# Kernel optimization log

Hardware: AMD Instinct MI355X
Metric: run time of the kernel (lower is better)

The kernel has to match this reference:

```python
import jax, jax.numpy as jnp
import numpy as np

N_Q = 8
DIM = 2 ** N_Q          # 256
DEGREE = 3
ANSATZ_LAYERS = 2


def gelu(x):
    return jax.nn.gelu(x, approximate=False)


def layer_norm(x, g, b, eps=1e-5):
    mu = x.mean(-1, keepdims=True)
    v = x.var(-1, keepdims=True)
    return (x - mu) / jnp.sqrt(v + eps) * g + b


def apply_ry(state, theta, w, n):
    # state: (B, 2^n) complex64, theta: (B,) per-element angle
    half = theta * 0.5
    c, s = jnp.cos(half), jnp.sin(half)
    U = jnp.stack([jnp.stack([c, -s], -1), jnp.stack([s, c], -1)], -2).astype(state.dtype)
    L, R = 2 ** w, 2 ** (n - 1 - w)
    st = state.reshape(-1, L, 2, R)
    st = jnp.einsum('bij,bljr->blir', U, st)
    return st.reshape(state.shape)


def apply_crx(state, theta, c, t, n):
    # controlled-RX(theta), control wire c, target wire t (batched angles)
    half = theta * 0.5
    cs = jnp.cos(half).astype(state.dtype)
    ms = (-1j) * jnp.sin(half).astype(state.dtype)
    Rx = jnp.stack([jnp.stack([cs, ms], -1), jnp.stack([ms, cs], -1)], -2)  # (B,2,2)
    a, b = min(c, t), max(c, t)
    A, M, R = 2 ** a, 2 ** (b - a - 1), 2 ** (n - 1 - b)
    st = state.reshape(-1, A, 2, M, 2, R)
    if c < t:
        sub = st[:, :, 1]                              # control bit = 1 slice, (B,A,M,2,R)
        sub = jnp.einsum('bij,bamjr->bamir', Rx, sub)
        st = st.at[:, :, 1].set(sub)
    else:
        sub = st[:, :, :, :, 1]                        # (B,A,2,M,R)
        sub = jnp.einsum('bij,bajmr->baimr', Rx, sub)
        st = st.at[:, :, :, :, 1].set(sub)
    return st.reshape(state.shape)


def sim14(state, params, n, layers):
    # Sim et al. 2019 circuit 14: RY layer, CRX ring, RY layer, reversed CRX ring (4n params/layer)
    idx = 0
    for _ in range(layers):
        for q in range(n):
            state = apply_ry(state, params[:, idx + q], q, n)
        idx += n
        for q in range(n):
            state = apply_crx(state, params[:, idx + q], q, (q + 1) % n, n)
        idx += n
        for q in range(n):
            state = apply_ry(state, params[:, idx + q], q, n)
        idx += n
        for q in range(n):
            state = apply_crx(state, params[:, idx + q], q, (q - 1) % n, n)
        idx += n
    return state


def pauli_expvals(psi, n):
    # [<X_0..X_{n-1}>, <Y_0..>, <Z_0..>] for batched pure states psi: (B, 2^n)
    xs, ys, zs = [], [], []
    for w in range(n):
        L, R = 2 ** w, 2 ** (n - 1 - w)
        s = psi.reshape(-1, L, 2, R)
        s0, s1 = s[:, :, 0], s[:, :, 1]
        cross = (jnp.conj(s0) * s1).sum((1, 2))
        xs.append(2.0 * jnp.real(cross))
        ys.append(2.0 * jnp.imag(cross))
        zs.append((jnp.abs(s0) ** 2 - jnp.abs(s1) ** 2).sum((1, 2)))
    return jnp.stack(xs + ys + zs, axis=1).astype(jnp.float32)


def dwsep_conv(x, dw_w, dw_b, pw_w, pw_b, gn_g, gn_b, dilation):
    # depthwise-separable conv1d + GroupNorm(8) + GELU; x: (B, C, T)
    k = dw_w.shape[-1]
    pad = (k - 1) * dilation // 2
    y = jax.lax.conv_general_dilated(
        x, dw_w, window_strides=(1,), padding=[(pad, pad)], rhs_dilation=(dilation,),
        feature_group_count=x.shape[1], dimension_numbers=('NCH', 'OIH', 'NCH'))
    y = y + dw_b[None, :, None]
    y = jnp.einsum('oc,bct->bot', pw_w, y) + pw_b[None, :, None]
    B, C, T = y.shape
    g = y.reshape(B, 8, C // 8, T)
    mu = g.mean((2, 3), keepdims=True)
    var = g.var((2, 3), keepdims=True)
    y = ((g - mu) / jnp.sqrt(var + 1e-5)).reshape(B, C, T)
    return gelu(y * gn_g[None, :, None] + gn_b[None, :, None])


def setup_inputs() -> dict:
    key = jax.random.key(0)
    ks = iter(jax.random.split(key, 64))
    rn = lambda *s: jax.random.normal(next(ks), s, jnp.float32) * 0.05
    ru = lambda *s: jax.random.uniform(next(ks), s, dtype=jnp.float32)
    inp = dict(
        x=jax.random.normal(next(ks), (16, 363, 180), jnp.float32),
        net_w=rn(12, 15, 8), net_b=rn(12, 8),
        dwa_w=rn(96, 1, 7), dwa_b=rn(96), pwa_w=rn(96, 96), pwa_b=rn(96),
        gna_g=jnp.ones(96, jnp.float32), gna_b=jnp.zeros(96, jnp.float32),
        dwb_w=rn(96, 1, 7), dwb_b=rn(96), pwb_w=rn(96, 96), pwb_b=rn(96),
        gnb_g=jnp.ones(96, jnp.float32), gnb_b=jnp.zeros(96, jnp.float32),
        dwc_w=rn(96, 1, 7), dwc_b=rn(96), pwc_w=rn(96, 96), pwc_b=rn(96),
        gnc_g=jnp.ones(96, jnp.float32), gnc_b=jnp.zeros(96, jnp.float32),
        merge_w=rn(288, 128), merge_b=rn(128),
        merge_ln_g=jnp.ones(128, jnp.float32), merge_ln_b=jnp.zeros(128, jnp.float32),
        qproj_w=rn(128, 64), qproj_b=rn(64),
        poly_coeffs=ru(4), qff_params=ru(32),
        mix_re=ru(363), mix_im=ru(363),
        qout_w=rn(24, 128), qout_b=rn(128),
        fc_w=rn(78, 64), fc_b=rn(64),
        fus1_w=rn(192, 128), fus1_b=rn(128),
        fus_ln_g=jnp.ones(128, jnp.float32), fus_ln_b=jnp.zeros(128, jnp.float32),
        fus2_w=rn(128, 64), fus2_b=rn(64),
    )
    return inp


def reference(x, net_w, net_b, dwa_w, dwa_b, pwa_w, pwa_b, gna_g, gna_b,
              dwb_w, dwb_b, pwb_w, pwb_b, gnb_g, gnb_b,
              dwc_w, dwc_b, pwc_w, pwc_b, gnc_g, gnc_b,
              merge_w, merge_b, merge_ln_g, merge_ln_b,
              qproj_w, qproj_b, poly_coeffs, qff_params, mix_re, mix_im,
              qout_w, qout_b, fc_w, fc_b,
              fus1_w, fus1_b, fus_ln_g, fus_ln_b, fus2_w, fus2_b):
    B, T, C = x.shape
    # --- network projection: 12 contiguous networks of 15 ROIs -> d_net=8 each ---
    h = jnp.einsum('btki,kid->btkd', x.reshape(B, T, 12, 15), net_w) + net_b
    h = gelu(h).reshape(B, T, 96)
    # --- multiscale depthwise-separable convs ---
    ht = h.transpose(0, 2, 1)  # (B,96,T)
    a = dwsep_conv(ht, dwa_w, dwa_b, pwa_w, pwa_b, gna_g, gna_b, 1)
    b = dwsep_conv(ht, dwb_w, dwb_b, pwb_w, pwb_b, gnb_g, gnb_b, 4)
    c = dwsep_conv(ht, dwc_w, dwc_b, pwc_w, pwc_b, gnc_g, gnc_b, 16)
    cat = jnp.concatenate([a, b, c], axis=1).transpose(0, 2, 1)  # (B,T,288)
    h = gelu(layer_norm(cat @ merge_w + merge_b, merge_ln_g, merge_ln_b))  # (B,T,128)
    # --- QSVT quantum temporal mixing ---
    tp = jax.nn.sigmoid(h @ qproj_w + qproj_b) * (2.0 * np.pi)  # (B,T,64) rotation angles
    tp = tp.reshape(B * T, -1)
    base = jnp.zeros((B * T, DIM), jnp.complex64).at[:, 0].set(1.0)
    pc = poly_coeffs.astype(jnp.complex64)
    state = base
    acc = pc[0] * base
    for d in range(1, DEGREE + 1):
        state = sim14(state, tp, N_Q, ANSATZ_LAYERS)
        acc = acc + pc[d] * state
    acc = acc.reshape(B, T, DIM)
    mix = (mix_re + 1j * mix_im).astype(jnp.complex64)[:T]
    mixed = jnp.einsum('t,btd->bd', mix, acc)           # temporal mixing
    norm = jnp.linalg.norm(mixed, axis=1, keepdims=True)
    psi = mixed / (norm + 1e-9)
    psi = sim14(psi, jnp.broadcast_to(qff_params[None, :], (B, qff_params.shape[0])), N_Q, 1)
    exps = pauli_expvals(psi, N_Q)                      # (B,24)
    temporal = exps @ qout_w + qout_b                   # (B,128)
    # --- FC fingerprint ---
    xm = x - x.mean(1, keepdims=True)
    std = jnp.maximum(jnp.std(x, axis=1, keepdims=True, ddof=1), 1e-8)
    xn = xm / std
    corr = jnp.einsum('btc,btd->bcd', xn, xn) / (T - 1)
    bm = corr.reshape(B, 12, 15, 12, 15).mean((2, 4))   # (B,12,12) network-block means
    iu0, iu1 = jnp.triu_indices(12)
    fc_vec = bm[:, iu0, iu1]                            # (B,78)
    fc = gelu(fc_vec @ fc_w + fc_b)                     # (B,64)
    # --- fusion ---
    fused = jnp.concatenate([temporal, fc], axis=1)
    out = gelu(layer_norm(fused @ fus1_w + fus1_b, fus_ln_g, fus_ln_b)) @ fus2_w + fus2_b
    return out  # (B,64)
```

## Files before the change

kernel.cpp:

```cpp
#include <hip/hip_runtime.h>
#include <math.h>

#define NB 16
#define NT 363
#define NC 180
#define SZF 557568
#define NROW 5808

__device__ __forceinline__ float gelu_f(float x) {
  return 0.5f * x * (1.0f + erff(x * 0.7071067811865475244f));
}


template<int CTRL>
__device__ __forceinline__ float dppf(float x) {
  return __int_as_float(__builtin_amdgcn_update_dpp(
      0, __float_as_int(x), CTRL, 0xF, 0xF, true));
}

template<int LB>
__device__ __forceinline__ float lx(float x) {
  if constexpr (LB == 0) return dppf<0xB1>(x);
  else if constexpr (LB == 1) return dppf<0x4E>(x);
  else if constexpr (LB == 2) return __shfl_xor(x, 4);
  else return __shfl_xor(x, 8);
}

template<int P>
__device__ __forceinline__ void ry_local(float* re, float* im, float c, float s) {
#pragma unroll
  for (int j = 0; j < 16; ++j) {
    if ((j & (1 << P)) == 0) {
      int k = j | (1 << P);
      float r0 = re[j], i0 = im[j], r1 = re[k], i1 = im[k];
      re[j] = fmaf(c, r0, -s * r1); im[j] = fmaf(c, i0, -s * i1);
      re[k] = fmaf(s, r0,  c * r1); im[k] = fmaf(s, i0,  c * i1);
    }
  }
}

template<int LB>
__device__ __forceinline__ void ry_lane(float* re, float* im, float c, float s, int lane) {
  float sg = (lane & (1 << LB)) ? s : -s;
#pragma unroll
  for (int j = 0; j < 16; ++j) {
    float br = lx<LB>(re[j]);
    float bi = lx<LB>(im[j]);
    re[j] = fmaf(c, re[j], sg * br);
    im[j] = fmaf(c, im[j], sg * bi);
  }
}

template<int Q, int P>
__device__ __forceinline__ void crx_ll(float* re, float* im, float cs, float sn) {
#pragma unroll
  for (int j = 0; j < 16; ++j) {
    if ((j & (1 << Q)) && !(j & (1 << P))) {
      int k = j | (1 << P);
      float r0 = re[j], i0 = im[j], r1 = re[k], i1 = im[k];
      re[j] = fmaf(cs, r0,  sn * i1); im[j] = fmaf(cs, i0, -sn * r1);
      re[k] = fmaf(cs, r1,  sn * i0); im[k] = fmaf(cs, i1, -sn * r0);
    }
  }
}

template<int LBQ, int P>
__device__ __forceinline__ void crx_nl(float* re, float* im, float cs, float sn, int lane) {
  if (lane & (1 << LBQ)) {
#pragma unroll
    for (int j = 0; j < 16; ++j) {
      if ((j & (1 << P)) == 0) {
        int k = j | (1 << P);
        float r0 = re[j], i0 = im[j], r1 = re[k], i1 = im[k];
        re[j] = fmaf(cs, r0,  sn * i1); im[j] = fmaf(cs, i0, -sn * r1);
        re[k] = fmaf(cs, r1,  sn * i0); im[k] = fmaf(cs, i1, -sn * r0);
      }
    }
  }
}

template<int Q, int LBP>
__device__ __forceinline__ void crx_ln(float* re, float* im, float cs, float sn) {
#pragma unroll
  for (int j = 0; j < 16; ++j) {
    if (j & (1 << Q)) {
      float br = lx<LBP>(re[j]);
      float bi = lx<LBP>(im[j]);
      re[j] = fmaf(cs, re[j],  sn * bi);
      im[j] = fmaf(cs, im[j], -sn * br);
    }
  }
}

template<int LBQ, int LBP>
__device__ __forceinline__ void crx_nn(float* re, float* im, float cs, float sn, int lane) {
  bool ctl = (lane & (1 << LBQ)) != 0;
#pragma unroll
  for (int j = 0; j < 16; ++j) {
    float br = lx<LBP>(re[j]);
    float bi = lx<LBP>(im[j]);
    if (ctl) {
      re[j] = fmaf(cs, re[j],  sn * bi);
      im[j] = fmaf(cs, im[j], -sn * br);
    }
  }
}

__device__ __forceinline__ void qlayer(float* re, float* im,
                                       const float2* ang, int lane) {
  float2 a;
  a = ang[0];  ry_lane<3>(re, im, a.x, a.y, lane);
  a = ang[1];  ry_lane<2>(re, im, a.x, a.y, lane);
  a = ang[2];  ry_lane<1>(re, im, a.x, a.y, lane);
  a = ang[3];  ry_lane<0>(re, im, a.x, a.y, lane);
  a = ang[4];  ry_local<3>(re, im, a.x, a.y);
  a = ang[5];  ry_local<2>(re, im, a.x, a.y);
  a = ang[6];  ry_local<1>(re, im, a.x, a.y);
  a = ang[7];  ry_local<0>(re, im, a.x, a.y);
  a = ang[8];  crx_nn<3, 2>(re, im, a.x, a.y, lane);
  a = ang[9];  crx_nn<2, 1>(re, im, a.x, a.y, lane);
  a = ang[10]; crx_nn<1, 0>(re, im, a.x, a.y, lane);
  a = ang[11]; crx_nl<0, 3>(re, im, a.x, a.y, lane);
  a = ang[12]; crx_ll<3, 2>(re, im, a.x, a.y);
  a = ang[13]; crx_ll<2, 1>(re, im, a.x, a.y);
  a = ang[14]; crx_ll<1, 0>(re, im, a.x, a.y);
  a = ang[15]; crx_ln<0, 3>(re, im, a.x, a.y);
  a = ang[16]; ry_lane<3>(re, im, a.x, a.y, lane);
  a = ang[17]; ry_lane<2>(re, im, a.x, a.y, lane);
  a = ang[18]; ry_lane<1>(re, im, a.x, a.y, lane);
  a = ang[19]; ry_lane<0>(re, im, a.x, a.y, lane);
  a = ang[20]; ry_local<3>(re, im, a.x, a.y);
  a = ang[21]; ry_local<2>(re, im, a.x, a.y);
  a = ang[22]; ry_local<1>(re, im, a.x, a.y);
  a = ang[23]; ry_local<0>(re, im, a.x, a.y);
  a = ang[24]; crx_nl<3, 0>(re, im, a.x, a.y, lane);
  a = ang[25]; crx_nn<2, 3>(re, im, a.x, a.y, lane);
  a = ang[26]; crx_nn<1, 2>(re, im, a.x, a.y, lane);
  a = ang[27]; crx_nn<0, 1>(re, im, a.x, a.y, lane);
  a = ang[28]; crx_ln<3, 0>(re, im, a.x, a.y);
  a = ang[29]; crx_ll<2, 3>(re, im, a.x, a.y);
  a = ang[30]; crx_ll<1, 2>(re, im, a.x, a.y);
  a = ang[31]; crx_ll<0, 1>(re, im, a.x, a.y);
}

template<int P>
__device__ __forceinline__ void ryg(float* re, float* im, float c, float s, int lane) {
  if constexpr (P >= 2) {
    constexpr int mask = 1 << (P - 2);
    float sg = ((lane >> (P - 2)) & 1) ? s : -s;
#pragma unroll
    for (int j = 0; j < 4; ++j) {
      float br = __shfl_xor(re[j], mask);
      float bi = __shfl_xor(im[j], mask);
      re[j] = fmaf(c, re[j], sg * br);
      im[j] = fmaf(c, im[j], sg * bi);
    }
  } else {
#pragma unroll
    for (int k = 0; k < 2; ++k) {
      const int a = (P == 0) ? 2 * k : k;
      const int b = (P == 0) ? a + 1 : a + 2;
      float r0 = re[a], i0 = im[a], r1 = re[b], i1 = im[b];
      re[a] = fmaf(c, r0, -s * r1); im[a] = fmaf(c, i0, -s * i1);
      re[b] = fmaf(s, r0,  c * r1); im[b] = fmaf(s, i0,  c * i1);
    }
  }
}

template<int PC, int PT>
__device__ __forceinline__ void crxg(float* re, float* im, float cs, float sn, int lane) {
  if constexpr (PT >= 2) {
    constexpr int mask = 1 << (PT - 2);
#pragma unroll
    for (int j = 0; j < 4; ++j) {
      float br = __shfl_xor(re[j], mask);
      float bi = __shfl_xor(im[j], mask);
      bool ctrl;
      if constexpr (PC >= 2) ctrl = ((lane >> (PC - 2)) & 1) != 0;
      else                   ctrl = ((j >> PC) & 1) != 0;
      if (ctrl) {
        float nr = fmaf(cs, re[j],  sn * bi);
        float ni = fmaf(cs, im[j], -sn * br);
        re[j] = nr; im[j] = ni;
      }
    }
  } else {
#pragma unroll
    for (int k = 0; k < 2; ++k) {
      const int a = (PT == 0) ? 2 * k : k;
      const int b = (PT == 0) ? a + 1 : a + 2;
      bool ctrl;
      if constexpr (PC >= 2) ctrl = ((lane >> (PC - 2)) & 1) != 0;
      else                   ctrl = ((a >> PC) & 1) != 0;
      if (ctrl) {
        float r0 = re[a], i0 = im[a], r1 = re[b], i1 = im[b];
        re[a] = fmaf(cs, r0,  sn * i1); im[a] = fmaf(cs, i0, -sn * r1);
        re[b] = fmaf(cs, r1,  sn * i0); im[b] = fmaf(cs, i1, -sn * r0);
      }
    }
  }
}

__device__ __forceinline__ void sim14_layer(float* re, float* im,
                                            const float* Cr, const float* Sr, int lane) {
#define ARY1(q, pi) ryg<7-(q)>(re, im, Cr[pi], Sr[pi], lane)
#define ACX1(cq, tq, pi) crxg<7-(cq), 7-(tq)>(re, im, Cr[pi], Sr[pi], lane)
  ARY1(0,0); ARY1(1,1); ARY1(2,2); ARY1(3,3); ARY1(4,4); ARY1(5,5); ARY1(6,6); ARY1(7,7);
  ACX1(0,1,8); ACX1(1,2,9); ACX1(2,3,10); ACX1(3,4,11); ACX1(4,5,12); ACX1(5,6,13); ACX1(6,7,14); ACX1(7,0,15);
  ARY1(0,16); ARY1(1,17); ARY1(2,18); ARY1(3,19); ARY1(4,20); ARY1(5,21); ARY1(6,22); ARY1(7,23);
  ACX1(0,7,24); ACX1(1,0,25); ACX1(2,1,26); ACX1(3,2,27); ACX1(4,3,28); ACX1(5,4,29); ACX1(6,5,30); ACX1(7,6,31);
#undef ARY1
#undef ACX1
}

struct CorrSM { float mu[180]; float inv[180]; float S[NT * 12]; float fcv[78]; };
struct EmdwSM {
  float xs[NT * 15];
  float nwL[120], nbL[8];
  float hrow[8][368];
  float wL[3][8][8];
  float bL[3][8];
};
union EDSM { EmdwSM e; CorrSM c; };

__global__ __launch_bounds__(256) void k_emdw(const float* __restrict__ x,
    const float* __restrict__ nw, const float* __restrict__ nb,
    const float* __restrict__ wa, const float* __restrict__ ba,
    const float* __restrict__ wb, const float* __restrict__ bb,
    const float* __restrict__ wc, const float* __restrict__ bc,
    float* __restrict__ y1base,
    const float* __restrict__ fcw, const float* __restrict__ fcb,
    float* __restrict__ fusedG) {
  __shared__ EDSM sm;
  int b = blockIdx.x, kg = blockIdx.y, tid = threadIdx.x;
  if (kg < 12) {
    for (int i = tid; i < 120; i += 256) sm.e.nwL[i] = nw[kg * 120 + i];
    for (int i = tid; i < 8; i += 256) sm.e.nbL[i] = nb[kg * 8 + i];
    for (int i = tid; i < 168; i += 256) {
      int z = i / 56, r = i % 56, d = r / 7, k = r % 7;
      const float* w = (z == 0) ? wa : ((z == 1) ? wb : wc);
      sm.e.wL[z][d][k] = w[(kg * 8 + d) * 7 + k];
    }
    for (int i = tid; i < 24; i += 256) {
      int z = i / 8, d = i % 8;
      const float* bias = (z == 0) ? ba : ((z == 1) ? bb : bc);
      sm.e.bL[z][d] = bias[kg * 8 + d];
    }
    for (int i = tid; i < NT * 15; i += 256) {
      int t = i / 15, u = i % 15;
      sm.e.xs[i] = x[((size_t)b * NT + t) * NC + kg * 15 + u];
    }
    __syncthreads();
    for (int i = tid; i < 8 * NT; i += 256) {
      int t = i % NT, d = i / NT;
      float acc2 = sm.e.nbL[d];
#pragma unroll
      for (int u = 0; u < 15; ++u) acc2 = fmaf(sm.e.xs[t * 15 + u], sm.e.nwL[u * 8 + d], acc2);
      sm.e.hrow[d][t] = gelu_f(acc2);
    }
    __syncthreads();
    for (int i = tid; i < 8 * NT; i += 256) {
      int t = i % NT, d = i / NT;
      int c = kg * 8 + d;
      float a0 = sm.e.bL[0][d], a1 = sm.e.bL[1][d], a2 = sm.e.bL[2][d];
#pragma unroll
      for (int k = 0; k < 7; ++k) {
        int i1 = t + (k - 3);
        int i4 = t + (k - 3) * 4;
        int i16 = t + (k - 3) * 16;
        if (i1 >= 0 && i1 < NT)  a0 = fmaf(sm.e.hrow[d][i1],  sm.e.wL[0][d][k], a0);
        if (i4 >= 0 && i4 < NT)  a1 = fmaf(sm.e.hrow[d][i4],  sm.e.wL[1][d][k], a1);
        if (i16 >= 0 && i16 < NT) a2 = fmaf(sm.e.hrow[d][i16], sm.e.wL[2][d][k], a2);
      }
      size_t base = ((size_t)b * 96 + c) * NT + t;
      y1base[base] = a0;
      y1base[SZF + base] = a1;
      y1base[2 * SZF + base] = a2;
    }
  } else {
    if (tid < 180) {
      float s = 0;
      const float* px = x + (size_t)b * NT * NC + tid;
      for (int t = 0; t < NT; ++t) s += px[t * NC];
      float mu = s / 363.0f;
      float q = 0;
      for (int t = 0; t < NT; ++t) { float d = px[t * NC] - mu; q = fmaf(d, d, q); }
      float sd = sqrtf(q / 362.0f);
      sd = fmaxf(sd, 1e-8f);
      sm.c.mu[tid] = mu; sm.c.inv[tid] = 1.0f / sd;
    }
    __syncthreads();
    for (int t = tid; t < NT; t += 256) {
      const float* px = x + (size_t)(b * NT + t) * NC;
#pragma unroll
      for (int i = 0; i < 12; ++i) {
        float s = 0;
#pragma unroll
        for (int u = 0; u < 15; ++u) {
          int cidx = i * 15 + u;
          s += (px[cidx] - sm.c.mu[cidx]) * sm.c.inv[cidx];
        }
        sm.c.S[t * 12 + i] = s;
      }
    }
    __syncthreads();
    if (tid < 78) {
      int i = 0, rem = tid;
      while (rem >= 12 - i) { rem -= 12 - i; ++i; }
      int j = i + rem;
      float acc = 0;
      for (int t = 0; t < NT; ++t) acc = fmaf(sm.c.S[t * 12 + i], sm.c.S[t * 12 + j], acc);
      sm.c.fcv[tid] = acc * (1.0f / (225.0f * 362.0f));
    }
    __syncthreads();
    if (tid < 64) {
      float v = fcb[tid];
#pragma unroll
      for (int k = 0; k < 78; ++k) v = fmaf(sm.c.fcv[k], fcw[k * 64 + tid], v);
      fusedG[b * 192 + 128 + tid] = gelu_f(v);
    }
  }
}

__global__ __launch_bounds__(256) void k_pw(const float* __restrict__ y1base,
    const float* __restrict__ wA, const float* __restrict__ wB, const float* __restrict__ wC,
    const float* __restrict__ bA, const float* __restrict__ bB, const float* __restrict__ bC,
    float* __restrict__ y2base) {
  int b = blockIdx.x, tile = blockIdx.y, z = blockIdx.z, tid = threadIdx.x;
  const float* pw_w = (z == 0) ? wA : ((z == 1) ? wB : wC);
  const float* pw_b = (z == 0) ? bA : ((z == 1) ? bB : bC);
  const float* y1 = y1base + (size_t)z * SZF;
  float* y2 = y2base + (size_t)z * SZF;
  int t0 = tile * 64;
  __shared__ float y1t[96 * 64];
  __shared__ float pwL[96 * 97];
  for (int i = tid; i < 96 * 96; i += 256) {
    int o = i / 96, cc = i % 96;
    pwL[o * 97 + cc] = pw_w[i];
  }
  for (int i = tid; i < 96 * 64; i += 256) {
    int cc = i >> 6, t = i & 63;
    int tt = t0 + t;
    y1t[i] = (tt < NT) ? y1[(b * 96 + cc) * NT + tt] : 0.0f;
  }
  __syncthreads();
  int o16 = tid >> 4, t4 = (tid & 15) * 4;
  for (int pass = 0; pass < 6; ++pass) {
    int o = pass * 16 + o16;
    float bias = pw_b[o];
    float a0 = bias, a1 = bias, a2 = bias, a3 = bias;
    const float* wrow = &pwL[o * 97];
#pragma unroll 4
    for (int cc = 0; cc < 96; ++cc) {
      const float4 vy = *reinterpret_cast<const float4*>(&y1t[cc * 64 + t4]);
      float w = wrow[cc];
      a0 = fmaf(w, vy.x, a0); a1 = fmaf(w, vy.y, a1);
      a2 = fmaf(w, vy.z, a2); a3 = fmaf(w, vy.w, a3);
    }
    int base = (b * 96 + o) * NT;
    int t = t0 + t4;
    if (t + 3 < NT) {
      y2[base + t] = a0; y2[base + t + 1] = a1; y2[base + t + 2] = a2; y2[base + t + 3] = a3;
    } else {
      if (t < NT) y2[base + t] = a0;
      if (t + 1 < NT) y2[base + t + 1] = a1;
      if (t + 2 < NT) y2[base + t + 2] = a2;
      if (t + 3 < NT) y2[base + t + 3] = a3;
    }
  }
}

__global__ __launch_bounds__(256) void k_gnstat(const float* __restrict__ y2base,
                                                float* __restrict__ muG,
                                                float* __restrict__ rsG) {
  int b = blockIdx.x, g = blockIdx.y, z = blockIdx.z, tid = threadIdx.x;
  __shared__ float red[256];
  const float* base = y2base + (size_t)z * SZF + (b * 96 + g * 12) * NT;
  float s = 0;
  for (int i = tid; i < 12 * NT; i += 256) s += base[i];
  red[tid] = s; __syncthreads();
  for (int st = 128; st > 0; st >>= 1) { if (tid < st) red[tid] += red[tid + st]; __syncthreads(); }
  float mu = red[0] / 4356.0f;
  __syncthreads();
  float q = 0;
  for (int i = tid; i < 12 * NT; i += 256) { float d = base[i] - mu; q = fmaf(d, d, q); }
  red[tid] = q; __syncthreads();
  for (int st = 128; st > 0; st >>= 1) { if (tid < st) red[tid] += red[tid + st]; __syncthreads(); }
  if (tid == 0) {
    float var = red[0] / 4356.0f;
    muG[(z * NB + b) * 8 + g] = mu;
    rsG[(z * NB + b) * 8 + g] = rsqrtf(var + 1e-5f);
  }
}

__global__ __launch_bounds__(256) void k_gnapply(const float* __restrict__ y2base,
    const float* __restrict__ muG, const float* __restrict__ rsG,
    const float* __restrict__ gA, const float* __restrict__ gB, const float* __restrict__ gC,
    const float* __restrict__ bA, const float* __restrict__ bB, const float* __restrict__ bC,
    float* __restrict__ cat) {
  int b = blockIdx.x, tile = blockIdx.y, z = blockIdx.z, tid = threadIdx.x;
  const float* gng = (z == 0) ? gA : ((z == 1) ? gB : gC);
  const float* gnb = (z == 0) ? bA : ((z == 1) ? bB : bC);
  const float* y2 = y2base + (size_t)z * SZF;
  int t0 = tile * 64;
  __shared__ float yL[96 * 65];
  __shared__ float muL[8], rsL[8];
  if (tid < 8) { muL[tid] = muG[(z * NB + b) * 8 + tid]; rsL[tid] = rsG[(z * NB + b) * 8 + tid]; }
  for (int i = tid; i < 96 * 64; i += 256) {
    int cc = i >> 6, t = i & 63;
    int tt = t0 + t;
    yL[cc * 65 + t] = (tt < NT) ? y2[(b * 96 + cc) * NT + tt] : 0.0f;
  }
  __syncthreads();
  for (int i = tid; i < 64 * 96; i += 256) {
    int tt = i / 96, cc = i % 96;
    int t = t0 + tt;
    if (t < NT) {
      int g = cc / 12;
      float v = (yL[cc * 65 + tt] - muL[g]) * rsL[g] * gng[cc] + gnb[cc];
      cat[((size_t)b * NT + t) * 288 + z * 96 + cc] = gelu_f(v);
    }
  }
}

__global__ __launch_bounds__(256) void k_merge(const float* __restrict__ cat,
    const float* __restrict__ mw, const float* __restrict__ mb,
    const float* __restrict__ lng, const float* __restrict__ lnb,
    const float* __restrict__ qw, const float* __restrict__ qb,
    float2* __restrict__ angG) {
  int blk = blockIdx.x, tid = threadIdx.x;
  __shared__ float catL[8][288];
  __shared__ float vL[8][129];
  __shared__ float hL[8][129];
  __shared__ float muS[8], rsS[8];
  for (int i = tid; i < 8 * 288; i += 256) {
    int r = i / 288, k = i % 288;
    catL[r][k] = cat[((size_t)blk * 8 + r) * 288 + k];
  }
  __syncthreads();
  int jj = tid & 127, rg = tid >> 7;
  float bias = mb[jj];
  float acc[4] = {bias, bias, bias, bias};
  for (int k = 0; k < 288; ++k) {
    float w = mw[k * 128 + jj];
#pragma unroll
    for (int r = 0; r < 4; ++r) acc[r] = fmaf(catL[rg * 4 + r][k], w, acc[r]);
  }
#pragma unroll
  for (int r = 0; r < 4; ++r) vL[rg * 4 + r][jj] = acc[r];
  __syncthreads();
  if (tid < 8) {
    float s = 0;
    for (int k = 0; k < 128; ++k) s += vL[tid][k];
    float mu = s / 128.0f;
    float q = 0;
    for (int k = 0; k < 128; ++k) { float d = vL[tid][k] - mu; q = fmaf(d, d, q); }
    muS[tid] = mu;
    rsS[tid] = rsqrtf(q / 128.0f + 1e-5f);
  }
  __syncthreads();
  float g = lng[jj], bb2 = lnb[jj];
#pragma unroll
  for (int r = 0; r < 4; ++r) {
    int row = rg * 4 + r;
    float h = (acc[r] - muS[row]) * rsS[row] * g + bb2;
    hL[row][jj] = gelu_f(h);
  }
  __syncthreads();
  int o = tid & 63;
  int r0 = (tid >> 6) * 2;
  for (int rr = 0; rr < 2; ++rr) {
    int row = r0 + rr;
    float u = qb[o];
    for (int k = 0; k < 128; ++k) u = fmaf(hL[row][k], qw[k * 64 + o], u);
    float tp = 6.2831853071795864769f / (1.0f + expf(-u));
    float hf = tp * 0.5f;
    int grow = blk * 8 + row;
    angG[(size_t)grow * 64 + o] = make_float2(cosf(hf), sinf(hf));
  }
}

__global__ __launch_bounds__(64) void k_quantum(const float2* __restrict__ angG,
                                                const float* __restrict__ pc4,
                                                float* __restrict__ accG) {
  const int lane = threadIdx.x;
  const int g = lane >> 4;
  const int ll = lane & 15;
  const int row0 = blockIdx.x * 4;
  __shared__ float2 angL[4][66];
#pragma unroll
  for (int q = 0; q < 4; ++q)
    angL[q][lane] = angG[(size_t)(row0 + q) * 64 + lane];
  __syncthreads();
  float p0 = pc4[0], p1 = pc4[1], p2 = pc4[2], p3 = pc4[3];
  float re[16], im[16];
#pragma unroll
  for (int j = 0; j < 16; ++j) { re[j] = 0.0f; im[j] = 0.0f; }
  if (ll == 0) re[0] = p3;
  const float2* ang = &angL[g][0];
  for (int rep = 0; rep < 3; ++rep) {
    qlayer(re, im, ang, lane);
    qlayer(re, im, ang + 32, lane);
    float pc = (rep == 0) ? p2 : (rep == 1) ? p1 : p0;
    if (ll == 0) re[0] += pc;
  }
  int row = row0 + g;
  float4* dst = reinterpret_cast<float4*>(accG + ((size_t)row * 256 + ll * 16) * 2);
#pragma unroll
  for (int h = 0; h < 8; ++h)
    dst[h] = make_float4(re[2 * h], im[2 * h], re[2 * h + 1], im[2 * h + 1]);
}

__global__ __launch_bounds__(256) void k_mix1(const float* __restrict__ accG,
                                              const float* __restrict__ mr,
                                              const float* __restrict__ mi,
                                              float* __restrict__ part) {
  int b = blockIdx.x, ch = blockIdx.y, d = threadIdx.x;
  int t0 = ch * 33;
  float sr = 0, si = 0;
  for (int i = 0; i < 33; ++i) {
    int t = t0 + i;
    const float2 a = *reinterpret_cast<const float2*>(accG + (size_t)((b * NT + t) * 256 + d) * 2);
    float m_r = mr[t], m_i = mi[t];
    sr = fmaf(m_r, a.x, fmaf(-m_i, a.y, sr));
    si = fmaf(m_r, a.y, fmaf(m_i, a.x, si));
  }
  float2* o = reinterpret_cast<float2*>(part + (size_t)((b * 11 + ch) * 256 + d) * 2);
  *o = make_float2(sr, si);
}

__global__ __launch_bounds__(256) void k_tail(const float* __restrict__ part,
    const float* __restrict__ qff,
    const float* __restrict__ qout_w, const float* __restrict__ qout_b,
    const float* __restrict__ fusedG,
    const float* __restrict__ w1, const float* __restrict__ b1,
    const float* __restrict__ lng, const float* __restrict__ lnb,
    const float* __restrict__ w2, const float* __restrict__ b2,
    float* __restrict__ out) {
  int b = blockIdx.x, tid = threadIdx.x;
  __shared__ float psiL[256][2];
  __shared__ float red[256];
  __shared__ float qcL[32], qsL[32], exps[24];
  __shared__ float tL[128], cL[64], hL[128];
  {
    float sr = 0, si = 0;
    for (int ch = 0; ch < 11; ++ch) {
      const float2 a = *reinterpret_cast<const float2*>(part + (size_t)((b * 11 + ch) * 256 + tid) * 2);
      sr += a.x; si += a.y;
    }
    psiL[tid][0] = sr; psiL[tid][1] = si;
    red[tid] = sr * sr + si * si;
  }
  if (tid < 32) { float h = qff[tid] * 0.5f; qcL[tid] = cosf(h); qsL[tid] = sinf(h); }
  __syncthreads();
  for (int s2 = 128; s2 > 0; s2 >>= 1) { if (tid < s2) red[tid] += red[tid + s2]; __syncthreads(); }
  float inv = 1.0f / (sqrtf(red[0]) + 1e-9f);
  __syncthreads();
  if (tid < 64) {
    int lane = tid;
    float re[4], im[4];
#pragma unroll
    for (int j = 0; j < 4; ++j) {
      re[j] = psiL[lane * 4 + j][0] * inv;
      im[j] = psiL[lane * 4 + j][1] * inv;
    }
    sim14_layer(re, im, qcL, qsL, lane);
#pragma unroll
    for (int j = 0; j < 4; ++j) { psiL[lane * 4 + j][0] = re[j]; psiL[lane * 4 + j][1] = im[j]; }
  }
  __syncthreads();
  if (tid < 64) {
    int lane = tid;
    for (int w = 0; w < 8; ++w) {
      int p = 7 - w;
      float cr = 0, ci = 0, z = 0;
#pragma unroll
      for (int k = 0; k < 2; ++k) {
        int pr = lane + k * 64;
        int lowmask = (1 << p) - 1;
        int i0 = ((pr >> p) << (p + 1)) | (pr & lowmask);
        int i1 = i0 | (1 << p);
        float r0 = psiL[i0][0], I0 = psiL[i0][1], r1 = psiL[i1][0], I1 = psiL[i1][1];
        cr += r0 * r1 + I0 * I1;
        ci += r0 * I1 - I0 * r1;
        z += r0 * r0 + I0 * I0 - r1 * r1 - I1 * I1;
      }
      for (int off = 32; off > 0; off >>= 1) {
        cr += __shfl_down(cr, off);
        ci += __shfl_down(ci, off);
        z  += __shfl_down(z, off);
      }
      if (lane == 0) { exps[w] = 2.0f * cr; exps[8 + w] = 2.0f * ci; exps[16 + w] = z; }
    }
  }
  __syncthreads();
  if (tid < 128) {
    float v = qout_b[tid];
#pragma unroll
    for (int k = 0; k < 24; ++k) v = fmaf(exps[k], qout_w[k * 128 + tid], v);
    tL[tid] = v;
  } else if (tid < 192) {
    cL[tid - 128] = fusedG[b * 192 + 128 + (tid - 128)];
  }
  __syncthreads();
  float v = 0.0f;
  if (tid < 128) {
    v = b1[tid];
    for (int k = 0; k < 128; ++k) v = fmaf(tL[k], w1[k * 128 + tid], v);
    for (int k = 0; k < 64; ++k)  v = fmaf(cL[k], w1[(128 + k) * 128 + tid], v);
    red[tid] = v;
  }
  __syncthreads();
  for (int s = 64; s > 0; s >>= 1) { if (tid < s) red[tid] += red[tid + s]; __syncthreads(); }
  float mu = red[0] / 128.0f;
  __syncthreads();
  float dv = v - mu;
  if (tid < 128) red[tid] = dv * dv;
  __syncthreads();
  for (int s = 64; s > 0; s >>= 1) { if (tid < s) red[tid] += red[tid + s]; __syncthreads(); }
  float var = red[0] / 128.0f;
  if (tid < 128) hL[tid] = gelu_f(dv * rsqrtf(var + 1e-5f) * lng[tid] + lnb[tid]);
  __syncthreads();
  if (tid < 64) {
    float o = b2[tid];
    for (int k = 0; k < 128; ++k) o = fmaf(hL[k], w2[k * 64 + tid], o);
    out[b * 64 + tid] = o;
  }
}

extern "C" void kernel_launch(void* const* d_in, const int* in_sizes, int n_in,
                              void* d_out, int out_size, void* d_ws, size_t ws_size,
                              hipStream_t stream) {
  const float* x       = (const float*)d_in[0];
  const float* net_w   = (const float*)d_in[1];
  const float* net_b   = (const float*)d_in[2];
  const float* dwa_w   = (const float*)d_in[3];
  const float* dwa_b   = (const float*)d_in[4];
  const float* pwa_w   = (const float*)d_in[5];
  const float* pwa_b   = (const float*)d_in[6];
  const float* gna_g   = (const float*)d_in[7];
  const float* gna_b   = (const float*)d_in[8];
  const float* dwb_w   = (const float*)d_in[9];
  const float* dwb_b   = (const float*)d_in[10];
  const float* pwb_w   = (const float*)d_in[11];
  const float* pwb_b   = (const float*)d_in[12];
  const float* gnb_g   = (const float*)d_in[13];
  const float* gnb_b   = (const float*)d_in[14];
  const float* dwc_w   = (const float*)d_in[15];
  const float* dwc_b   = (const float*)d_in[16];
  const float* pwc_w   = (const float*)d_in[17];
  const float* pwc_b   = (const float*)d_in[18];
  const float* gnc_g   = (const float*)d_in[19];
  const float* gnc_b   = (const float*)d_in[20];
  const float* merge_w = (const float*)d_in[21];
  const float* merge_b = (const float*)d_in[22];
  const float* mlng    = (const float*)d_in[23];
  const float* mlnb    = (const float*)d_in[24];
  const float* qproj_w = (const float*)d_in[25];
  const float* qproj_b = (const float*)d_in[26];
  const float* poly    = (const float*)d_in[27];
  const float* qff     = (const float*)d_in[28];
  const float* mix_re  = (const float*)d_in[29];
  const float* mix_im  = (const float*)d_in[30];
  const float* qout_w  = (const float*)d_in[31];
  const float* qout_b  = (const float*)d_in[32];
  const float* fc_w    = (const float*)d_in[33];
  const float* fc_b    = (const float*)d_in[34];
  const float* fus1_w  = (const float*)d_in[35];
  const float* fus1_b  = (const float*)d_in[36];
  const float* flng    = (const float*)d_in[37];
  const float* flnb    = (const float*)d_in[38];
  const float* fus2_w  = (const float*)d_in[39];
  const float* fus2_b  = (const float*)d_in[40];
  float* out = (float*)d_out;

  float* W = (float*)d_ws;
  float* y1b_  = W;
  float* cat   = W;
  float* y2b_  = W + 3 * (size_t)SZF;
  float* acc   = W;
  float2* angG = (float2*)(W + 6 * (size_t)SZF);
  float* muG   = W + 6 * (size_t)SZF + 743424;
  float* rsG   = muG + 512;
  float* part  = rsG + 512;
  float* fused = part + 90112;

  k_emdw<<<dim3(NB, 13), 256, 0, stream>>>(x, net_w, net_b,
      dwa_w, dwa_b, dwb_w, dwb_b, dwc_w, dwc_b, y1b_, fc_w, fc_b, fused);
  k_pw<<<dim3(NB, 6, 3), 256, 0, stream>>>(y1b_, pwa_w, pwb_w, pwc_w, pwa_b, pwb_b, pwc_b, y2b_);
  k_gnstat<<<dim3(NB, 8, 3), 256, 0, stream>>>(y2b_, muG, rsG);
  k_gnapply<<<dim3(NB, 6, 3), 256, 0, stream>>>(y2b_, muG, rsG,
      gna_g, gnb_g, gnc_g, gna_b, gnb_b, gnc_b, cat);
  k_merge<<<726, 256, 0, stream>>>(cat, merge_w, merge_b, mlng, mlnb,
      qproj_w, qproj_b, angG);
  k_quantum<<<NROW / 4, 64, 0, stream>>>(angG, poly, acc);
  k_mix1<<<dim3(NB, 11), 256, 0, stream>>>(acc, mix_re, mix_im, part);
  k_tail<<<NB, 256, 0, stream>>>(part, qff, qout_w, qout_b, fused,
                                 fus1_w, fus1_b, flng, flnb, fus2_w, fus2_b, out);
}
```

Measured before the change: 316.8 us.

## Fuse group-norm stats into pointwise conv and temporal mixing into quantum kernel

GroupNorm statistics are now built in the pointwise conv kernel as per-group sum and sum-of-squares using wave shuffles and atomics, with buffers zeroed in the first kernel. This removes the separate stats kernel and its re-read of y2. The quantum kernel also applies the complex temporal mixing weight and reduces four time steps in-register before writing partial sums, so the full per-timestep state buffer and the mix kernel go away. In exchange, the tail kernel sums 91 partials instead of 11, variance uses E[x^2]-mu^2, which is less numerically stable, and atomic summation order is nondeterministic.

```diff
diff --git a/kernel.cpp b/kernel.cpp
--- a/kernel.cpp
+++ b/kernel.cpp
@@ -230,7 +230,8 @@
     const float* __restrict__ wc, const float* __restrict__ bc,
     float* __restrict__ y1base,
     const float* __restrict__ fcw, const float* __restrict__ fcb,
-    float* __restrict__ fusedG) {
+    float* __restrict__ fusedG,
+    float* __restrict__ statS, float* __restrict__ statQ) {
   __shared__ EDSM sm;
   int b = blockIdx.x, kg = blockIdx.y, tid = threadIdx.x;
   if (kg < 12) {
@@ -278,6 +279,11 @@
       y1base[2 * SZF + base] = a2;
     }
   } else {
+    if (tid < 24) {
+      int z = tid / 8, g = tid % 8;
+      statS[(z * NB + b) * 8 + g] = 0.0f;
+      statQ[(z * NB + b) * 8 + g] = 0.0f;
+    }
     if (tid < 180) {
       float s = 0;
       const float* px = x + (size_t)b * NT * NC + tid;
@@ -325,7 +331,8 @@
 __global__ __launch_bounds__(256) void k_pw(const float* __restrict__ y1base,
     const float* __restrict__ wA, const float* __restrict__ wB, const float* __restrict__ wC,
     const float* __restrict__ bA, const float* __restrict__ bB, const float* __restrict__ bC,
-    float* __restrict__ y2base) {
+    float* __restrict__ y2base,
+    float* __restrict__ statS, float* __restrict__ statQ) {
   int b = blockIdx.x, tile = blockIdx.y, z = blockIdx.z, tid = threadIdx.x;
   const float* pw_w = (z == 0) ? wA : ((z == 1) ? wB : wC);
   const float* pw_b = (z == 0) ? bA : ((z == 1) ? bB : bC);
@@ -367,34 +374,26 @@
       if (t + 2 < NT) y2[base + t + 2] = a2;
       if (t + 3 < NT) y2[base + t + 3] = a3;
     }
-  }
-}
-
-__global__ __launch_bounds__(256) void k_gnstat(const float* __restrict__ y2base,
-                                                float* __restrict__ muG,
-                                                float* __restrict__ rsG) {
-  int b = blockIdx.x, g = blockIdx.y, z = blockIdx.z, tid = threadIdx.x;
-  __shared__ float red[256];
-  const float* base = y2base + (size_t)z * SZF + (b * 96 + g * 12) * NT;
-  float s = 0;
-  for (int i = tid; i < 12 * NT; i += 256) s += base[i];
-  red[tid] = s; __syncthreads();
-  for (int st = 128; st > 0; st >>= 1) { if (tid < st) red[tid] += red[tid + st]; __syncthreads(); }
-  float mu = red[0] / 4356.0f;
-  __syncthreads();
-  float q = 0;
-  for (int i = tid; i < 12 * NT; i += 256) { float d = base[i] - mu; q = fmaf(d, d, q); }
-  red[tid] = q; __syncthreads();
-  for (int st = 128; st > 0; st >>= 1) { if (tid < st) red[tid] += red[tid + st]; __syncthreads(); }
-  if (tid == 0) {
-    float var = red[0] / 4356.0f;
-    muG[(z * NB + b) * 8 + g] = mu;
-    rsG[(z * NB + b) * 8 + g] = rsqrtf(var + 1e-5f);
+    float s = 0.0f, q = 0.0f;
+    if (t < NT)     { s += a0; q = fmaf(a0, a0, q); }
+    if (t + 1 < NT) { s += a1; q = fmaf(a1, a1, q); }
+    if (t + 2 < NT) { s += a2; q = fmaf(a2, a2, q); }
+    if (t + 3 < NT) { s += a3; q = fmaf(a3, a3, q); }
+#pragma unroll
+    for (int m = 1; m <= 8; m <<= 1) {
+      s += __shfl_xor(s, m);
+      q += __shfl_xor(q, m);
+    }
+    if ((tid & 15) == 0) {
+      int g = o / 12;
+      atomicAdd(&statS[(z * NB + b) * 8 + g], s);
+      atomicAdd(&statQ[(z * NB + b) * 8 + g], q);
+    }
   }
 }
 
 __global__ __launch_bounds__(256) void k_gnapply(const float* __restrict__ y2base,
-    const float* __restrict__ muG, const float* __restrict__ rsG,
+    const float* __restrict__ statS, const float* __restrict__ statQ,
     const float* __restrict__ gA, const float* __restrict__ gB, const float* __restrict__ gC,
     const float* __restrict__ bA, const float* __restrict__ bB, const float* __restrict__ bC,
     float* __restrict__ cat) {
@@ -405,7 +404,14 @@
   int t0 = tile * 64;
   __shared__ float yL[96 * 65];
   __shared__ float muL[8], rsL[8];
-  if (tid < 8) { muL[tid] = muG[(z * NB + b) * 8 + tid]; rsL[tid] = rsG[(z * NB + b) * 8 + tid]; }
+  if (tid < 8) {
+    float S = statS[(z * NB + b) * 8 + tid];
+    float Q = statQ[(z * NB + b) * 8 + tid];
+    float mu = S / 4356.0f;
+    float var = Q / 4356.0f - mu * mu;
+    muL[tid] = mu;
+    rsL[tid] = rsqrtf(fmaxf(var, 0.0f) + 1e-5f);
+  }
   for (int i = tid; i < 96 * 64; i += 256) {
     int cc = i >> 6, t = i & 63;
     int tt = t0 + t;
@@ -482,15 +488,21 @@
 
 __global__ __launch_bounds__(64) void k_quantum(const float2* __restrict__ angG,
                                                 const float* __restrict__ pc4,
-                                                float* __restrict__ accG) {
+                                                const float* __restrict__ mr,
+                                                const float* __restrict__ mi,
+                                                float* __restrict__ part) {
   const int lane = threadIdx.x;
   const int g = lane >> 4;
   const int ll = lane & 15;
-  const int row0 = blockIdx.x * 4;
+  const int b = blockIdx.x;
+  const int i = blockIdx.y;
   __shared__ float2 angL[4][66];
 #pragma unroll
-  for (int q = 0; q < 4; ++q)
-    angL[q][lane] = angG[(size_t)(row0 + q) * 64 + lane];
+  for (int q = 0; q < 4; ++q) {
+    int t = i * 4 + q;
+    if (t >= NT) t = NT - 1;
+    angL[q][lane] = angG[(size_t)(b * NT + t) * 64 + lane];
+  }
   __syncthreads();
   float p0 = pc4[0], p1 = pc4[1], p2 = pc4[2], p3 = pc4[3];
   float re[16], im[16];
@@ -504,29 +516,30 @@
     float pc = (rep == 0) ? p2 : (rep == 1) ? p1 : p0;
     if (ll == 0) re[0] += pc;
   }
-  int row = row0 + g;
-  float4* dst = reinterpret_cast<float4*>(accG + ((size_t)row * 256 + ll * 16) * 2);
-#pragma unroll
-  for (int h = 0; h < 8; ++h)
-    dst[h] = make_float4(re[2 * h], im[2 * h], re[2 * h + 1], im[2 * h + 1]);
-}
-
-__global__ __launch_bounds__(256) void k_mix1(const float* __restrict__ accG,
-                                              const float* __restrict__ mr,
-                                              const float* __restrict__ mi,
-                                              float* __restrict__ part) {
-  int b = blockIdx.x, ch = blockIdx.y, d = threadIdx.x;
-  int t0 = ch * 33;
-  float sr = 0, si = 0;
-  for (int i = 0; i < 33; ++i) {
-    int t = t0 + i;
-    const float2 a = *reinterpret_cast<const float2*>(accG + (size_t)((b * NT + t) * 256 + d) * 2);
-    float m_r = mr[t], m_i = mi[t];
-    sr = fmaf(m_r, a.x, fmaf(-m_i, a.y, sr));
-    si = fmaf(m_r, a.y, fmaf(m_i, a.x, si));
-  }
-  float2* o = reinterpret_cast<float2*>(part + (size_t)((b * 11 + ch) * 256 + d) * 2);
-  *o = make_float2(sr, si);
+  {
+    int t = i * 4 + g;
+    float m_r = 0.0f, m_i = 0.0f;
+    if (t < NT) { m_r = mr[t]; m_i = mi[t]; }
+#pragma unroll
+    for (int j = 0; j < 16; ++j) {
+      float r = re[j], v = im[j];
+      re[j] = m_r * r - m_i * v;
+      im[j] = m_r * v + m_i * r;
+    }
+#pragma unroll
+    for (int j = 0; j < 16; ++j) {
+      re[j] += __shfl_xor(re[j], 16);
+      im[j] += __shfl_xor(im[j], 16);
+      re[j] += __shfl_xor(re[j], 32);
+      im[j] += __shfl_xor(im[j], 32);
+    }
+  }
+  if (g == 0) {
+    float4* dst = reinterpret_cast<float4*>(part + ((size_t)(b * 91 + i) * 256 + ll * 16) * 2);
+#pragma unroll
+    for (int h = 0; h < 8; ++h)
+      dst[h] = make_float4(re[2 * h], im[2 * h], re[2 * h + 1], im[2 * h + 1]);
+  }
 }
 
 __global__ __launch_bounds__(256) void k_tail(const float* __restrict__ part,
@@ -543,9 +556,10 @@
   __shared__ float qcL[32], qsL[32], exps[24];
   __shared__ float tL[128], cL[64], hL[128];
   {
+    const float2* pv = reinterpret_cast<const float2*>(part) + (size_t)(b * 91) * 256 + tid;
     float sr = 0, si = 0;
-    for (int ch = 0; ch < 11; ++ch) {
-      const float2 a = *reinterpret_cast<const float2*>(part + (size_t)((b * 11 + ch) * 256 + tid) * 2);
+    for (int i = 0; i < 91; ++i) {
+      float2 a = pv[(size_t)i * 256];
       sr += a.x; si += a.y;
     }
     psiL[tid][0] = sr; psiL[tid][1] = si;
@@ -678,23 +692,21 @@
   float* y1b_  = W;
   float* cat   = W;
   float* y2b_  = W + 3 * (size_t)SZF;
-  float* acc   = W;
   float2* angG = (float2*)(W + 6 * (size_t)SZF);
-  float* muG   = W + 6 * (size_t)SZF + 743424;
-  float* rsG   = muG + 512;
-  float* part  = rsG + 512;
-  float* fused = part + 90112;
+  float* statS = W + 6 * (size_t)SZF + 743424;
+  float* statQ = statS + 384;
+  float* part  = statQ + 384;
+  float* fused = part + 745472;
 
   k_emdw<<<dim3(NB, 13), 256, 0, stream>>>(x, net_w, net_b,
-      dwa_w, dwa_b, dwb_w, dwb_b, dwc_w, dwc_b, y1b_, fc_w, fc_b, fused);
-  k_pw<<<dim3(NB, 6, 3), 256, 0, stream>>>(y1b_, pwa_w, pwb_w, pwc_w, pwa_b, pwb_b, pwc_b, y2b_);
-  k_gnstat<<<dim3(NB, 8, 3), 256, 0, stream>>>(y2b_, muG, rsG);
-  k_gnapply<<<dim3(NB, 6, 3), 256, 0, stream>>>(y2b_, muG, rsG,
+      dwa_w, dwa_b, dwb_w, dwb_b, dwc_w, dwc_b, y1b_, fc_w, fc_b, fused, statS, statQ);
+  k_pw<<<dim3(NB, 6, 3), 256, 0, stream>>>(y1b_, pwa_w, pwb_w, pwc_w, pwa_b, pwb_b, pwc_b,
+      y2b_, statS, statQ);
+  k_gnapply<<<dim3(NB, 6, 3), 256, 0, stream>>>(y2b_, statS, statQ,
       gna_g, gnb_g, gnc_g, gna_b, gnb_b, gnc_b, cat);
   k_merge<<<726, 256, 0, stream>>>(cat, merge_w, merge_b, mlng, mlnb,
       qproj_w, qproj_b, angG);
-  k_quantum<<<NROW / 4, 64, 0, stream>>>(angG, poly, acc);
-  k_mix1<<<dim3(NB, 11), 256, 0, stream>>>(acc, mix_re, mix_im, part);
+  k_quantum<<<dim3(NB, 91), 64, 0, stream>>>(angG, poly, mix_re, mix_im, part);
   k_tail<<<NB, 256, 0, stream>>>(part, qff, qout_w, qout_b, fused,
                                  fus1_w, fus1_b, flng, flnb, fus2_w, fus2_b, out);
 }
```

After: 326.8 us. 3.2% more time.
